# Kernel tuning notes

Hardware: AMD Instinct MI355X
Metric: run time of the kernel (lower is better)

## Reference

```python
import jax, jax.numpy as jnp
import numpy as np

N_NODES = 100000
N_EDGES = 1600000


def gcn_conv(x, W, b, src, dst, n):
    # PyG GCNConv: x @ W, add self-loops, symmetric deg^{-1/2} normalization,
    # sum-aggregate messages from src into dst, then add bias.
    h = x @ W  # [N, out]
    loops = jnp.arange(n, dtype=src.dtype)
    s = jnp.concatenate([src, loops])
    d = jnp.concatenate([dst, loops])
    deg = jax.ops.segment_sum(jnp.ones_like(d, dtype=h.dtype), d, num_segments=n)
    dinv = 1.0 / jnp.sqrt(deg)  # deg >= 1 thanks to self-loops
    norm = dinv[s] * dinv[d]  # [E + N]
    msg = h[s] * norm[:, None]
    out = jax.ops.segment_sum(msg, d, num_segments=n)
    return out + b


def setup_inputs() -> dict:
    key = jax.random.key(0)
    k1, k2, k3, k4 = jax.random.split(key, 4)
    x = jax.random.normal(k1, (N_NODES, 64), dtype=jnp.float32)
    edge_index = jax.random.randint(k2, (2, N_EDGES), 0, N_NODES, dtype=jnp.int64)
    W1 = jax.random.normal(k3, (64, 32), dtype=jnp.float32) * (1.0 / np.sqrt(64))
    b1 = jnp.zeros((32,), dtype=jnp.float32)
    W2 = jax.random.normal(k4, (32, 16), dtype=jnp.float32) * (1.0 / np.sqrt(32))
    b2 = jnp.zeros((16,), dtype=jnp.float32)
    return {"x": x, "edge_index": edge_index, "W1": W1, "b1": b1, "W2": W2, "b2": b2}


def reference(x, edge_index, W1, b1, W2, b2):
    n = x.shape[0]
    src, dst = edge_index[0], edge_index[1]
    h = gcn_conv(x, W1, b1, src, dst, n)
    h = jax.nn.relu(h)
    h = gcn_conv(h, W2, b2, src, dst, n)
    return jax.nn.log_softmax(h, axis=1)
```

## Files before the change

### kernel.cpp

```cpp
#include <hip/hip_runtime.h>
#include <hip/hip_bf16.h>


#define FEAT_IN 64
#define FEAT_H  32
#define FEAT_O  16
#define MAXNB   512
#define PART_G  256
#define MAXSNB  128

__device__ __forceinline__ float2 upk_bf2(unsigned w) {
    return make_float2(__uint_as_float(w << 16), __uint_as_float(w & 0xFFFF0000u));
}

__global__ void k_hist(const int* __restrict__ dst, int e,
                       int* __restrict__ hist, int G, int NBk) {
    __shared__ int lh[MAXNB];
    int t = threadIdx.x, g = blockIdx.x;
    for (int i = t; i < NBk; i += 256) lh[i] = 0;
    __syncthreads();
    int chunk = (e + G - 1) / G;
    int beg = g * chunk, end = min(e, beg + chunk);
    for (int i = beg + t; i < end; i += 256) atomicAdd(&lh[dst[i] >> 8], 1);
    __syncthreads();
    for (int i = t; i < NBk; i += 256) hist[(size_t)i * G + g] = lh[i];
}

__global__ void k_scan1(const int* __restrict__ in, int* __restrict__ out,
                        int* __restrict__ bsum, int len) {
    __shared__ int s[256];
    int t = threadIdx.x;
    int base = blockIdx.x * 1024 + t * 4;
    int a0 = (base + 0) < len ? in[base + 0] : 0;
    int a1 = (base + 1) < len ? in[base + 1] : 0;
    int a2 = (base + 2) < len ? in[base + 2] : 0;
    int a3 = (base + 3) < len ? in[base + 3] : 0;
    int tsum = a0 + a1 + a2 + a3;
    s[t] = tsum;
    __syncthreads();
    for (int off = 1; off < 256; off <<= 1) {
        int x = (t >= off) ? s[t - off] : 0;
        __syncthreads();
        s[t] += x;
        __syncthreads();
    }
    int ex = s[t] - tsum;
    if (base + 0 < len) out[base + 0] = ex;
    if (base + 1 < len) out[base + 1] = ex + a0;
    if (base + 2 < len) out[base + 2] = ex + a0 + a1;
    if (base + 3 < len) out[base + 3] = ex + a0 + a1 + a2;
    if (t == 255) bsum[blockIdx.x] = s[255];
}

__device__ __forceinline__ void scan_bsum(const int* __restrict__ bsum, int snb,
                                          int* __restrict__ sps, int t) {
    if (t < snb) sps[t] = bsum[t];
    __syncthreads();
    if (t == 0) {
        int acc = 0;
        for (int i = 0; i < snb; ++i) { int v = sps[i]; sps[i] = acc; acc += v; }
    }
    __syncthreads();
}

__global__ void k_partition(const int* __restrict__ src, const int* __restrict__ dst, int e,
                            const int* __restrict__ base, const int* __restrict__ bsum,
                            int snb, int* __restrict__ part, int G, int NBk) {
    __shared__ int cur[MAXNB];
    __shared__ int sps[MAXSNB];
    int t = threadIdx.x, g = blockIdx.x;
    scan_bsum(bsum, snb, sps, t);
    for (int i = t; i < NBk; i += 256) {
        size_t idx = (size_t)i * G + g;
        cur[i] = base[idx] + sps[idx >> 10];
    }
    __syncthreads();
    int chunk = (e + G - 1) / G;
    int beg = g * chunk, end = min(e, beg + chunk);
    for (int i = beg + t; i < end; i += 256) {
        int s_ = src[i], d_ = dst[i];
        int pos = atomicAdd(&cur[d_ >> 8], 1);
        part[pos] = s_ | ((d_ & 255) << 24);
    }
}

__global__ void k_bucket_csr(const int* __restrict__ part, const int* __restrict__ base,
                             const int* __restrict__ bsum, int snb, int e, int G, int NBk,
                             int n, int* __restrict__ row_start, int* __restrict__ col,
                             float* __restrict__ dinv) {
    __shared__ int cnt[256], spre[256], cur[256], ssc[256];
    __shared__ int sps[MAXSNB];
    int t = threadIdx.x, b = blockIdx.x;
    scan_bsum(bsum, snb, sps, t);
    size_t ib = (size_t)b * G;
    size_t ie = (size_t)(b + 1) * G;
    int beg = base[ib] + sps[ib >> 10];
    int end = (b == NBk - 1) ? e : (base[ie] + sps[ie >> 10]);
    cnt[t] = 0; cur[t] = 0;
    __syncthreads();
    for (int j = beg + t; j < end; j += 256) atomicAdd(&cnt[((unsigned)part[j]) >> 24], 1);
    __syncthreads();
    int v = cnt[t];
    ssc[t] = v;
    __syncthreads();
    for (int off = 1; off < 256; off <<= 1) {
        int x = (t >= off) ? ssc[t - off] : 0;
        __syncthreads();
        ssc[t] += x;
        __syncthreads();
    }
    spre[t] = ssc[t] - v;
    int node = b * 256 + t;
    if (node < n) {
        row_start[node] = beg + spre[t];
        dinv[node] = rsqrtf((float)v + 1.0f);
    }
    if (b == NBk - 1 && t == 0) row_start[n] = e;
    __syncthreads();
    for (int j = beg + t; j < end; j += 256) {
        int r = part[j];
        int dl = ((unsigned)r) >> 24;
        int off = atomicAdd(&cur[dl], 1);
        col[beg + spre[dl] + off] = r & 0x00FFFFFF;
    }
}

__global__ void k_gemm1(const float* __restrict__ x, const float* __restrict__ W1,
                        const float* __restrict__ dinv,
                        __hip_bfloat162* __restrict__ h1s2, int n) {
    __shared__ float sW[FEAT_IN * FEAT_H];
    __shared__ float sx[16][FEAT_IN + 1];
    int t = threadIdx.x;
    for (int i = t; i < FEAT_IN * FEAT_H; i += 256) sW[i] = W1[i];
#pragma unroll
    for (int tile = 0; tile < 2; ++tile) {
        int nodeBase = blockIdx.x * 32 + tile * 16;
        __syncthreads();
        {
            int xn = t >> 4, c = t & 15;
            int node = nodeBase + xn;
            if (node < n) {
                float4 v = ((const float4*)x)[(size_t)node * 16 + c];
                sx[xn][c * 4 + 0] = v.x; sx[xn][c * 4 + 1] = v.y;
                sx[xn][c * 4 + 2] = v.z; sx[xn][c * 4 + 3] = v.w;
            }
        }
        __syncthreads();
        int nl = t >> 4, g = t & 15;
        int node = nodeBase + nl;
        if (node < n) {
            float a0 = 0.0f, a1 = 0.0f;
#pragma unroll
            for (int k = 0; k < FEAT_IN; ++k) {
                float s = sx[nl][k];
                a0 += s * sW[k * FEAT_H + 2 * g];
                a1 += s * sW[k * FEAT_H + 2 * g + 1];
            }
            float dv = dinv[node];
            __hip_bfloat162 o;
            o.x = __float2bfloat16(a0 * dv);
            o.y = __float2bfloat16(a1 * dv);
            h1s2[(size_t)node * 16 + g] = o;
        }
    }
}

#define ACC8(u) do { float2 p_;                         \
    p_ = upk_bf2((u).x); a[0] += p_.x; a[1] += p_.y;    \
    p_ = upk_bf2((u).y); a[2] += p_.x; a[3] += p_.y;    \
    p_ = upk_bf2((u).z); a[4] += p_.x; a[5] += p_.y;    \
    p_ = upk_bf2((u).w); a[6] += p_.x; a[7] += p_.y; } while (0)

__global__ void k_gather1_gemm2(const int* __restrict__ row_start, const int* __restrict__ col,
                                const uint4* __restrict__ h1q, const float* __restrict__ W2,
                                const float* __restrict__ b1,
                                const float* __restrict__ dinv,
                                __hip_bfloat162* __restrict__ h2s2, int n) {
    __shared__ float sW[FEAT_H * FEAT_O];
    __shared__ float sb1[FEAT_H];
    __shared__ float sz[64][FEAT_H + 1];
    int t = threadIdx.x;
    for (int i = t; i < FEAT_H * FEAT_O; i += 256) sW[i] = W2[i];
    if (t < FEAT_H) sb1[t] = b1[t];
    __syncthreads();

    int g = t >> 2, l = t & 3;
    int d = blockIdx.x * 64 + g;
    if (d < n) {
        float a[8];
        {
            uint4 u = h1q[(size_t)d * 4 + l];
            float2 p;
            p = upk_bf2(u.x); a[0] = p.x; a[1] = p.y;
            p = upk_bf2(u.y); a[2] = p.x; a[3] = p.y;
            p = upk_bf2(u.z); a[4] = p.x; a[5] = p.y;
            p = upk_bf2(u.w); a[6] = p.x; a[7] = p.y;
        }
        int beg = row_start[d], end = row_start[d + 1];
        int j = beg;
        for (; j + 8 <= end; j += 8) {
            int c0 = col[j + 0], c1 = col[j + 1], c2 = col[j + 2], c3 = col[j + 3];
            int c4 = col[j + 4], c5 = col[j + 5], c6 = col[j + 6], c7 = col[j + 7];
            uint4 u0 = h1q[(size_t)c0 * 4 + l];
            uint4 u1 = h1q[(size_t)c1 * 4 + l];
            uint4 u2 = h1q[(size_t)c2 * 4 + l];
            uint4 u3 = h1q[(size_t)c3 * 4 + l];
            uint4 u4 = h1q[(size_t)c4 * 4 + l];
            uint4 u5 = h1q[(size_t)c5 * 4 + l];
            uint4 u6 = h1q[(size_t)c6 * 4 + l];
            uint4 u7 = h1q[(size_t)c7 * 4 + l];
            ACC8(u0); ACC8(u1); ACC8(u2); ACC8(u3);
            ACC8(u4); ACC8(u5); ACC8(u6); ACC8(u7);
        }
        for (; j + 4 <= end; j += 4) {
            int c0 = col[j + 0], c1 = col[j + 1], c2 = col[j + 2], c3 = col[j + 3];
            uint4 u0 = h1q[(size_t)c0 * 4 + l];
            uint4 u1 = h1q[(size_t)c1 * 4 + l];
            uint4 u2 = h1q[(size_t)c2 * 4 + l];
            uint4 u3 = h1q[(size_t)c3 * 4 + l];
            ACC8(u0); ACC8(u1); ACC8(u2); ACC8(u3);
        }
        for (; j < end; ++j) {
            uint4 u = h1q[(size_t)col[j] * 4 + l];
            ACC8(u);
        }
        float dv = dinv[d];
#pragma unroll
        for (int k = 0; k < 8; ++k)
            sz[g][l * 8 + k] = fmaxf(dv * a[k] + sb1[l * 8 + k], 0.0f);
    }
    __syncthreads();
#pragma unroll
    for (int it = 0; it < 2; ++it) {
        int nl = (t >> 3) + it * 32;
        int m = t & 7;
        int node = blockIdx.x * 64 + nl;
        if (node < n) {
            float a0 = 0.0f, a1 = 0.0f;
#pragma unroll
            for (int f = 0; f < FEAT_H; ++f) {
                float z = sz[nl][f];
                a0 += z * sW[f * FEAT_O + 2 * m];
                a1 += z * sW[f * FEAT_O + 2 * m + 1];
            }
            float dv = dinv[node];
            __hip_bfloat162 o;
            o.x = __float2bfloat16(a0 * dv);
            o.y = __float2bfloat16(a1 * dv);
            h2s2[(size_t)node * 8 + m] = o;
        }
    }
}

__global__ void k_gather2_lsm(const int* __restrict__ row_start, const int* __restrict__ col,
                              const uint4* __restrict__ h2q, const float* __restrict__ b2,
                              const float* __restrict__ dinv,
                              float4* __restrict__ out4, int n) {
    __shared__ float sb2[FEAT_O];
    int t = threadIdx.x;
    if (t < FEAT_O) sb2[t] = b2[t];
    __syncthreads();
    int g = t >> 1, h = t & 1;
    int d = blockIdx.x * 128 + g;
    if (d >= n) return;
    float a[8];
    {
        uint4 u = h2q[(size_t)d * 2 + h];
        float2 p;
        p = upk_bf2(u.x); a[0] = p.x; a[1] = p.y;
        p = upk_bf2(u.y); a[2] = p.x; a[3] = p.y;
        p = upk_bf2(u.z); a[4] = p.x; a[5] = p.y;
        p = upk_bf2(u.w); a[6] = p.x; a[7] = p.y;
    }
    int beg = row_start[d], end = row_start[d + 1];
    int j = beg;
    for (; j + 8 <= end; j += 8) {
        int c0 = col[j + 0], c1 = col[j + 1], c2 = col[j + 2], c3 = col[j + 3];
        int c4 = col[j + 4], c5 = col[j + 5], c6 = col[j + 6], c7 = col[j + 7];
        uint4 u0 = h2q[(size_t)c0 * 2 + h];
        uint4 u1 = h2q[(size_t)c1 * 2 + h];
        uint4 u2 = h2q[(size_t)c2 * 2 + h];
        uint4 u3 = h2q[(size_t)c3 * 2 + h];
        uint4 u4 = h2q[(size_t)c4 * 2 + h];
        uint4 u5 = h2q[(size_t)c5 * 2 + h];
        uint4 u6 = h2q[(size_t)c6 * 2 + h];
        uint4 u7 = h2q[(size_t)c7 * 2 + h];
        ACC8(u0); ACC8(u1); ACC8(u2); ACC8(u3);
        ACC8(u4); ACC8(u5); ACC8(u6); ACC8(u7);
    }
    for (; j + 4 <= end; j += 4) {
        int c0 = col[j + 0], c1 = col[j + 1], c2 = col[j + 2], c3 = col[j + 3];
        uint4 u0 = h2q[(size_t)c0 * 2 + h];
        uint4 u1 = h2q[(size_t)c1 * 2 + h];
        uint4 u2 = h2q[(size_t)c2 * 2 + h];
        uint4 u3 = h2q[(size_t)c3 * 2 + h];
        ACC8(u0); ACC8(u1); ACC8(u2); ACC8(u3);
    }
    for (; j < end; ++j) {
        uint4 u = h2q[(size_t)col[j] * 2 + h];
        ACC8(u);
    }
    float dv = dinv[d];
    float v[8];
    float mx = -1e30f;
#pragma unroll
    for (int k = 0; k < 8; ++k) {
        v[k] = dv * a[k] + sb2[h * 8 + k];
        mx = fmaxf(mx, v[k]);
    }
    mx = fmaxf(mx, __shfl_xor(mx, 1));
    float ssum = 0.0f;
#pragma unroll
    for (int k = 0; k < 8; ++k) ssum += __expf(v[k] - mx);
    ssum += __shfl_xor(ssum, 1);
    float lg = mx + logf(ssum);
    float4 o0 = { v[0] - lg, v[1] - lg, v[2] - lg, v[3] - lg };
    float4 o1 = { v[4] - lg, v[5] - lg, v[6] - lg, v[7] - lg };
    out4[(size_t)d * 4 + h * 2 + 0] = o0;
    out4[(size_t)d * 4 + h * 2 + 1] = o1;
}

extern "C" void kernel_launch(void* const* d_in, const int* in_sizes, int n_in,
                              void* d_out, int out_size, void* d_ws, size_t ws_size,
                              hipStream_t stream) {
    const float* x  = (const float*)d_in[0];
    const int*   ei = (const int*)d_in[1];
    const float* W1 = (const float*)d_in[2];
    const float* b1 = (const float*)d_in[3];
    const float* W2 = (const float*)d_in[4];
    const float* b2 = (const float*)d_in[5];

    const int n = in_sizes[0] / FEAT_IN;
    const int e = in_sizes[1] / 2;
    const int* src = ei;
    const int* dst = ei + e;
    const int NBk = (n + 255) >> 8;
    const int G = PART_G;
    const int hlen = NBk * G;
    const int snb = (hlen + 1023) / 1024;

    int* part = (int*)d_ws;
    __hip_bfloat162* h1s2 = (__hip_bfloat162*)d_ws;
    int* col  = (int*)d_ws + e;
    __hip_bfloat162* h2s2 = (__hip_bfloat162*)(col + e);
    float* dinv = (float*)(h2s2 + 8 * (size_t)n);
    int* hist      = (int*)(dinv + n);
    int* base      = hist + hlen;
    int* bsum      = base + hlen;
    int* row_start = bsum + MAXSNB;

    k_hist<<<G, 256, 0, stream>>>(dst, e, hist, G, NBk);
    k_scan1<<<snb, 256, 0, stream>>>(hist, base, bsum, hlen);
    k_partition<<<G, 256, 0, stream>>>(src, dst, e, base, bsum, snb, part, G, NBk);
    k_bucket_csr<<<NBk, 256, 0, stream>>>(part, base, bsum, snb, e, G, NBk, n,
                                          row_start, col, dinv);

    k_gemm1<<<(n + 31) / 32, 256, 0, stream>>>(x, W1, dinv, h1s2, n);
    k_gather1_gemm2<<<(n + 63) / 64, 256, 0, stream>>>(row_start, col, (const uint4*)h1s2,
                                                       W2, b1, dinv, h2s2, n);
    k_gather2_lsm<<<(n + 127) / 128, 256, 0, stream>>>(row_start, col, (const uint4*)h2s2,
                                                       b2, dinv, (float4*)d_out, n);
}
```

Before: 184.6 us.

## Vectorize CSR build loads with int4 and double partition block count

The histogram, partition and bucket-CSR kernels now read dst, src and partitioned edges as int4 vectors, with 4-aligned chunks and scalar head and tail loops. The partition grid grows from 256 to 512 blocks, and the serial single-thread block-sum scan becomes a parallel shared-memory scan sized for the larger block count. This targets instruction and load overhead in the CSR construction kernels and adds parallelism. In exchange the code is more complex and there are more histogram entries to scan.

```diff
diff --git a/kernel.cpp b/kernel.cpp
--- a/kernel.cpp
+++ b/kernel.cpp
@@ -6,8 +6,8 @@
 #define FEAT_H  32
 #define FEAT_O  16
 #define MAXNB   512
-#define PART_G  256
-#define MAXSNB  128
+#define PART_G  512
+#define MAXSNB  256
 
 __device__ __forceinline__ float2 upk_bf2(unsigned w) {
     return make_float2(__uint_as_float(w << 16), __uint_as_float(w & 0xFFFF0000u));
@@ -19,9 +19,21 @@
     int t = threadIdx.x, g = blockIdx.x;
     for (int i = t; i < NBk; i += 256) lh[i] = 0;
     __syncthreads();
-    int chunk = (e + G - 1) / G;
+    int chunk = (((e + G - 1) / G) + 3) & ~3;
     int beg = g * chunk, end = min(e, beg + chunk);
-    for (int i = beg + t; i < end; i += 256) atomicAdd(&lh[dst[i] >> 8], 1);
+    if ((e & 3) == 0) {
+        int vend = beg + ((end - beg) & ~3);
+        for (int j = beg + 4 * t; j + 3 < vend; j += 1024) {
+            int4 d = *(const int4*)&dst[j];
+            atomicAdd(&lh[d.x >> 8], 1);
+            atomicAdd(&lh[d.y >> 8], 1);
+            atomicAdd(&lh[d.z >> 8], 1);
+            atomicAdd(&lh[d.w >> 8], 1);
+        }
+        for (int j = vend + t; j < end; j += 256) atomicAdd(&lh[dst[j] >> 8], 1);
+    } else {
+        for (int i = beg + t; i < end; i += 256) atomicAdd(&lh[dst[i] >> 8], 1);
+    }
     __syncthreads();
     for (int i = t; i < NBk; i += 256) hist[(size_t)i * G + g] = lh[i];
 }
@@ -54,12 +66,18 @@
 
 __device__ __forceinline__ void scan_bsum(const int* __restrict__ bsum, int snb,
                                           int* __restrict__ sps, int t) {
-    if (t < snb) sps[t] = bsum[t];
-    __syncthreads();
-    if (t == 0) {
-        int acc = 0;
-        for (int i = 0; i < snb; ++i) { int v = sps[i]; sps[i] = acc; acc += v; }
-    }
+    int v = (t < snb) ? bsum[t] : 0;
+    sps[t] = v;
+    __syncthreads();
+    for (int off = 1; off < 256; off <<= 1) {
+        int x = (t >= off) ? sps[t - off] : 0;
+        __syncthreads();
+        sps[t] += x;
+        __syncthreads();
+    }
+    int inc = sps[t];
+    __syncthreads();
+    sps[t] = inc - v;
     __syncthreads();
 }
 
@@ -75,12 +93,29 @@
         cur[i] = base[idx] + sps[idx >> 10];
     }
     __syncthreads();
-    int chunk = (e + G - 1) / G;
+    int chunk = (((e + G - 1) / G) + 3) & ~3;
     int beg = g * chunk, end = min(e, beg + chunk);
-    for (int i = beg + t; i < end; i += 256) {
-        int s_ = src[i], d_ = dst[i];
-        int pos = atomicAdd(&cur[d_ >> 8], 1);
-        part[pos] = s_ | ((d_ & 255) << 24);
+    if ((e & 3) == 0) {
+        int vend = beg + ((end - beg) & ~3);
+        for (int j = beg + 4 * t; j + 3 < vend; j += 1024) {
+            int4 s4 = *(const int4*)&src[j];
+            int4 d4 = *(const int4*)&dst[j];
+            int p0 = atomicAdd(&cur[d4.x >> 8], 1); part[p0] = s4.x | ((d4.x & 255) << 24);
+            int p1 = atomicAdd(&cur[d4.y >> 8], 1); part[p1] = s4.y | ((d4.y & 255) << 24);
+            int p2 = atomicAdd(&cur[d4.z >> 8], 1); part[p2] = s4.z | ((d4.z & 255) << 24);
+            int p3 = atomicAdd(&cur[d4.w >> 8], 1); part[p3] = s4.w | ((d4.w & 255) << 24);
+        }
+        for (int j = vend + t; j < end; j += 256) {
+            int s_ = src[j], d_ = dst[j];
+            int pos = atomicAdd(&cur[d_ >> 8], 1);
+            part[pos] = s_ | ((d_ & 255) << 24);
+        }
+    } else {
+        for (int i = beg + t; i < end; i += 256) {
+            int s_ = src[i], d_ = dst[i];
+            int pos = atomicAdd(&cur[d_ >> 8], 1);
+            part[pos] = s_ | ((d_ & 255) << 24);
+        }
     }
 }
 
@@ -98,7 +133,20 @@
     int end = (b == NBk - 1) ? e : (base[ie] + sps[ie >> 10]);
     cnt[t] = 0; cur[t] = 0;
     __syncthreads();
-    for (int j = beg + t; j < end; j += 256) atomicAdd(&cnt[((unsigned)part[j]) >> 24], 1);
+    {
+        int a0 = min(end, (beg + 3) & ~3);
+        if (t < a0 - beg) atomicAdd(&cnt[((unsigned)part[beg + t]) >> 24], 1);
+        for (int j = a0 + 4 * t; j + 3 < end; j += 1024) {
+            int4 r = *(const int4*)&part[j];
+            atomicAdd(&cnt[((unsigned)r.x) >> 24], 1);
+            atomicAdd(&cnt[((unsigned)r.y) >> 24], 1);
+            atomicAdd(&cnt[((unsigned)r.z) >> 24], 1);
+            atomicAdd(&cnt[((unsigned)r.w) >> 24], 1);
+        }
+        int vend = a0 + ((end - a0) & ~3);
+        for (int j = vend + t; j < end; j += 256)
+            atomicAdd(&cnt[((unsigned)part[j]) >> 24], 1);
+    }
     __syncthreads();
     int v = cnt[t];
     ssc[t] = v;
@@ -117,11 +165,33 @@
     }
     if (b == NBk - 1 && t == 0) row_start[n] = e;
     __syncthreads();
-    for (int j = beg + t; j < end; j += 256) {
-        int r = part[j];
-        int dl = ((unsigned)r) >> 24;
-        int off = atomicAdd(&cur[dl], 1);
-        col[beg + spre[dl] + off] = r & 0x00FFFFFF;
+    {
+        int a0 = min(end, (beg + 3) & ~3);
+        if (t < a0 - beg) {
+            int r = part[beg + t];
+            int dl = ((unsigned)r) >> 24;
+            int off = atomicAdd(&cur[dl], 1);
+            col[beg + spre[dl] + off] = r & 0x00FFFFFF;
+        }
+        for (int j = a0 + 4 * t; j + 3 < end; j += 1024) {
+            int4 r4 = *(const int4*)&part[j];
+            int dl, off;
+            dl = ((unsigned)r4.x) >> 24; off = atomicAdd(&cur[dl], 1);
+            col[beg + spre[dl] + off] = r4.x & 0x00FFFFFF;
+            dl = ((unsigned)r4.y) >> 24; off = atomicAdd(&cur[dl], 1);
+            col[beg + spre[dl] + off] = r4.y & 0x00FFFFFF;
+            dl = ((unsigned)r4.z) >> 24; off = atomicAdd(&cur[dl], 1);
+            col[beg + spre[dl] + off] = r4.z & 0x00FFFFFF;
+            dl = ((unsigned)r4.w) >> 24; off = atomicAdd(&cur[dl], 1);
+            col[beg + spre[dl] + off] = r4.w & 0x00FFFFFF;
+        }
+        int vend = a0 + ((end - a0) & ~3);
+        for (int j = vend + t; j < end; j += 256) {
+            int r = part[j];
+            int dl = ((unsigned)r) >> 24;
+            int off = atomicAdd(&cur[dl], 1);
+            col[beg + spre[dl] + off] = r & 0x00FFFFFF;
+        }
     }
 }
 
```

New measurement: 180.9 us. 2.0% less time.
